# Performance work log

Hardware: AMD Instinct MI355X
Metric: run time of the kernel (lower is better)

## Reference

```python
import jax, jax.numpy as jnp
import numpy as np

D = H = W = 128
NUM_STEPS = 7  # MONAI DVF2DDF default


def _base_grid(dtype):
    zz, yy, xx = jnp.meshgrid(jnp.arange(D, dtype=dtype),
                              jnp.arange(H, dtype=dtype),
                              jnp.arange(W, dtype=dtype), indexing='ij')
    return jnp.stack([zz, yy, xx], 0)  # [3,D,H,W] voxel coords


def _warp(img, ddf, mode):
    # img: [1,C,D,H,W], ddf: [1,3,D,H,W] in voxel units.
    # Equivalent to grid_sample(align_corners=True, padding='border'):
    # border padding == clamp the voxel-space sample coordinate to [0, dim-1].
    dtype = ddf.dtype
    coords = _base_grid(dtype) + ddf[0]
    lims = jnp.array([D - 1, H - 1, W - 1], dtype=dtype).reshape(3, 1, 1, 1)
    coords = jnp.clip(coords, 0.0, lims)
    vol = img[0]  # [C,D,H,W]
    if mode == 'nearest':
        zi, yi, xi = jnp.round(coords).astype(jnp.int32)
        return vol[:, zi, yi, xi][None]
    z, y, x = coords
    z0 = jnp.floor(z); y0 = jnp.floor(y); x0 = jnp.floor(x)
    wz = z - z0; wy = y - y0; wx = x - x0
    z0i = z0.astype(jnp.int32); y0i = y0.astype(jnp.int32); x0i = x0.astype(jnp.int32)
    z1i = jnp.minimum(z0i + 1, D - 1)
    y1i = jnp.minimum(y0i + 1, H - 1)
    x1i = jnp.minimum(x0i + 1, W - 1)
    g = lambda a, b, c: vol[:, a, b, c]  # [C,D,H,W] gather
    out = (g(z0i, y0i, x0i) * (1 - wz) * (1 - wy) * (1 - wx)
         + g(z0i, y0i, x1i) * (1 - wz) * (1 - wy) * wx
         + g(z0i, y1i, x0i) * (1 - wz) * wy * (1 - wx)
         + g(z0i, y1i, x1i) * (1 - wz) * wy * wx
         + g(z1i, y0i, x0i) * wz * (1 - wy) * (1 - wx)
         + g(z1i, y0i, x1i) * wz * (1 - wy) * wx
         + g(z1i, y1i, x0i) * wz * wy * (1 - wx)
         + g(z1i, y1i, x1i) * wz * wy * wx)
    return out[None]


def _dvf2ddf(dvf):
    # scaling-and-squaring integration of a stationary velocity field
    ddf = dvf / (2.0 ** NUM_STEPS)
    for _ in range(NUM_STEPS):
        ddf = ddf + _warp(ddf, ddf, 'bilinear')
    return ddf


def setup_inputs() -> dict:
    key = jax.random.key(0)
    k1, k2, k3, k4 = jax.random.split(key, 4)
    dvf = jax.random.normal(k1, (1, 3, D, H, W), dtype=jnp.float32) * 0.5
    moving_image = jax.random.uniform(k2, (1, 1, D, H, W), dtype=jnp.float32)
    fixed_image = jax.random.uniform(k3, (1, 1, D, H, W), dtype=jnp.float32)
    moving_label = jax.random.randint(k4, (1, 1, D, H, W), 0, 4).astype(jnp.float32)
    return {'dvf': dvf, 'moving_image': moving_image,
            'fixed_image': fixed_image, 'moving_label': moving_label}


def reference(dvf, moving_image, fixed_image, moving_label):
    ddf = _dvf2ddf(dvf)
    pred_image = _warp(moving_image, ddf, 'bilinear')
    pred_label = _warp(moving_label, ddf, 'nearest')
    return (ddf, pred_image, pred_label, dvf)
```

## Files before the change

kernel.cpp:

```cpp
#include <hip/hip_runtime.h>

#define DD 128
constexpr int NV = DD * DD * DD;
constexpr float INV_SCALE = 1.0f / 128.0f;

__device__ __forceinline__ void unpack_zyx(int tid, int& z, int& y, int& x) {
    x = tid & (DD - 1);
    y = (tid >> 7) & (DD - 1);
    z = tid >> 14;
}

__device__ __forceinline__ float clampd(float v) {
    return fminf(fmaxf(v, 0.0f), (float)(DD - 1));
}

struct Corner {
    int i000, i001, i010, i011, i100, i101, i110, i111;
    float w000, w001, w010, w011, w100, w101, w110, w111;
};

__device__ __forceinline__ Corner make_corner(float cz, float cy, float cx) {
    Corner c;
    float z0f = floorf(cz), y0f = floorf(cy), x0f = floorf(cx);
    float wz = cz - z0f, wy = cy - y0f, wx = cx - x0f;
    int z0 = (int)z0f, y0 = (int)y0f, x0 = (int)x0f;
    int dx = (x0 < DD - 1) ? 1 : 0;
    int dy = (y0 < DD - 1) ? DD : 0;
    int dz = (z0 < DD - 1) ? DD * DD : 0;
    int i000 = (z0 << 14) + (y0 << 7) + x0;
    c.i000 = i000;           c.i001 = i000 + dx;
    c.i010 = i000 + dy;      c.i011 = i000 + dy + dx;
    c.i100 = i000 + dz;      c.i101 = i000 + dz + dx;
    c.i110 = i000 + dz + dy; c.i111 = i000 + dz + dy + dx;
    float omz = 1.0f - wz, omy = 1.0f - wy, omx = 1.0f - wx;
    c.w000 = omz * omy * omx; c.w001 = omz * omy * wx;
    c.w010 = omz * wy * omx;  c.w011 = omz * wy * wx;
    c.w100 = wz * omy * omx;  c.w101 = wz * omy * wx;
    c.w110 = wz * wy * omx;   c.w111 = wz * wy * wx;
    return c;
}


__global__ __launch_bounds__(256)
void init_step1_kernel(const float* __restrict__ dvf,
                       float4* __restrict__ dst,
                       float* __restrict__ dvf_out) {
    int tid = blockIdx.x * blockDim.x + threadIdx.x;
    int z, y, x;
    unpack_zyx(tid, z, y, x);

    float v0 = dvf[tid];
    float v1 = dvf[tid + NV];
    float v2 = dvf[tid + 2 * NV];

    dvf_out[tid]          = v0;
    dvf_out[tid + NV]     = v1;
    dvf_out[tid + 2 * NV] = v2;

    float d0 = v0 * INV_SCALE, d1 = v1 * INV_SCALE, d2 = v2 * INV_SCALE;

    float cz = clampd((float)z + d0);
    float cy = clampd((float)y + d1);
    float cx = clampd((float)x + d2);

    Corner c = make_corner(cz, cy, cx);
    const float* ch0 = dvf;
    const float* ch1 = dvf + NV;
    const float* ch2 = dvf + 2 * NV;

    float t0 = c.w000 * ch0[c.i000] + c.w001 * ch0[c.i001]
             + c.w010 * ch0[c.i010] + c.w011 * ch0[c.i011]
             + c.w100 * ch0[c.i100] + c.w101 * ch0[c.i101]
             + c.w110 * ch0[c.i110] + c.w111 * ch0[c.i111];
    float t1 = c.w000 * ch1[c.i000] + c.w001 * ch1[c.i001]
             + c.w010 * ch1[c.i010] + c.w011 * ch1[c.i011]
             + c.w100 * ch1[c.i100] + c.w101 * ch1[c.i101]
             + c.w110 * ch1[c.i110] + c.w111 * ch1[c.i111];
    float t2 = c.w000 * ch2[c.i000] + c.w001 * ch2[c.i001]
             + c.w010 * ch2[c.i010] + c.w011 * ch2[c.i011]
             + c.w100 * ch2[c.i100] + c.w101 * ch2[c.i101]
             + c.w110 * ch2[c.i110] + c.w111 * ch2[c.i111];

    dst[tid] = make_float4(t0 * INV_SCALE + d0,
                           t1 * INV_SCALE + d1,
                           t2 * INV_SCALE + d2, 0.0f);
}

template <bool PLANAR_OUT>
__global__ __launch_bounds__(256)
void step4_kernel(const float4* __restrict__ src,
                  float4* __restrict__ dst4,
                  float* __restrict__ dstp) {
    int tid = blockIdx.x * blockDim.x + threadIdx.x;
    int z, y, x;
    unpack_zyx(tid, z, y, x);

    float4 d = src[tid];

    float cz = clampd((float)z + d.x);
    float cy = clampd((float)y + d.y);
    float cx = clampd((float)x + d.z);

    Corner c = make_corner(cz, cy, cx);

    float4 v000 = src[c.i000], v001 = src[c.i001];
    float4 v010 = src[c.i010], v011 = src[c.i011];
    float4 v100 = src[c.i100], v101 = src[c.i101];
    float4 v110 = src[c.i110], v111 = src[c.i111];

    float r0 = c.w000 * v000.x + c.w001 * v001.x + c.w010 * v010.x + c.w011 * v011.x
             + c.w100 * v100.x + c.w101 * v101.x + c.w110 * v110.x + c.w111 * v111.x;
    float r1 = c.w000 * v000.y + c.w001 * v001.y + c.w010 * v010.y + c.w011 * v011.y
             + c.w100 * v100.y + c.w101 * v101.y + c.w110 * v110.y + c.w111 * v111.y;
    float r2 = c.w000 * v000.z + c.w001 * v001.z + c.w010 * v010.z + c.w011 * v011.z
             + c.w100 * v100.z + c.w101 * v101.z + c.w110 * v110.z + c.w111 * v111.z;

    r0 += d.x; r1 += d.y; r2 += d.z;

    if (PLANAR_OUT) {
        dstp[tid]          = r0;
        dstp[tid + NV]     = r1;
        dstp[tid + 2 * NV] = r2;
    } else {
        dst4[tid] = make_float4(r0, r1, r2, 0.0f);
    }
}

__global__ __launch_bounds__(256)
void final_kernel(const float* __restrict__ ddf,
                  const float* __restrict__ mimg,
                  const float* __restrict__ mlab,
                  float* __restrict__ pred_img,
                  float* __restrict__ pred_lab) {
    int tid = blockIdx.x * blockDim.x + threadIdx.x;
    int z, y, x;
    unpack_zyx(tid, z, y, x);

    float d0 = ddf[tid];
    float d1 = ddf[tid + NV];
    float d2 = ddf[tid + 2 * NV];

    float cz = clampd((float)z + d0);
    float cy = clampd((float)y + d1);
    float cx = clampd((float)x + d2);

    Corner c = make_corner(cz, cy, cx);

    float v = c.w000 * mimg[c.i000] + c.w001 * mimg[c.i001]
            + c.w010 * mimg[c.i010] + c.w011 * mimg[c.i011]
            + c.w100 * mimg[c.i100] + c.w101 * mimg[c.i101]
            + c.w110 * mimg[c.i110] + c.w111 * mimg[c.i111];
    pred_img[tid] = v;

    int zi = (int)rintf(cz);
    int yi = (int)rintf(cy);
    int xi = (int)rintf(cx);
    pred_lab[tid] = mlab[(zi << 14) + (yi << 7) + xi];
}


__device__ __forceinline__ void trilerp3(const float* __restrict__ src,
                                         float cz, float cy, float cx,
                                         float& r0, float& r1, float& r2) {
    Corner c = make_corner(cz, cy, cx);
    const float* p000 = src + 3 * c.i000;
    const float* p001 = src + 3 * c.i001;
    const float* p010 = src + 3 * c.i010;
    const float* p011 = src + 3 * c.i011;
    const float* p100 = src + 3 * c.i100;
    const float* p101 = src + 3 * c.i101;
    const float* p110 = src + 3 * c.i110;
    const float* p111 = src + 3 * c.i111;
    r0 = c.w000 * p000[0] + c.w001 * p001[0] + c.w010 * p010[0] + c.w011 * p011[0]
       + c.w100 * p100[0] + c.w101 * p101[0] + c.w110 * p110[0] + c.w111 * p111[0];
    r1 = c.w000 * p000[1] + c.w001 * p001[1] + c.w010 * p010[1] + c.w011 * p011[1]
       + c.w100 * p100[1] + c.w101 * p101[1] + c.w110 * p110[1] + c.w111 * p111[1];
    r2 = c.w000 * p000[2] + c.w001 * p001[2] + c.w010 * p010[2] + c.w011 * p011[2]
       + c.w100 * p100[2] + c.w101 * p101[2] + c.w110 * p110[2] + c.w111 * p111[2];
}

__global__ __launch_bounds__(256)
void init_kernel(const float* __restrict__ dvf, float* __restrict__ A) {
    int tid = blockIdx.x * blockDim.x + threadIdx.x;
    float d0 = dvf[tid] * INV_SCALE;
    float d1 = dvf[tid + NV] * INV_SCALE;
    float d2 = dvf[tid + 2 * NV] * INV_SCALE;
    float* p = A + 3 * tid;
    p[0] = d0; p[1] = d1; p[2] = d2;
}

template <bool PLANAR_OUT>
__global__ __launch_bounds__(256)
void step_kernel(const float* __restrict__ src, float* __restrict__ dst) {
    int tid = blockIdx.x * blockDim.x + threadIdx.x;
    int z, y, x;
    unpack_zyx(tid, z, y, x);
    const float* s = src + 3 * tid;
    float d0 = s[0], d1 = s[1], d2 = s[2];
    float cz = clampd((float)z + d0);
    float cy = clampd((float)y + d1);
    float cx = clampd((float)x + d2);
    float r0, r1, r2;
    trilerp3(src, cz, cy, cx, r0, r1, r2);
    r0 += d0; r1 += d1; r2 += d2;
    if (PLANAR_OUT) {
        dst[tid]          = r0;
        dst[tid + NV]     = r1;
        dst[tid + 2 * NV] = r2;
    } else {
        float* p = dst + 3 * tid;
        p[0] = r0; p[1] = r1; p[2] = r2;
    }
}

__global__ __launch_bounds__(256)
void final_kernel_fb(const float* __restrict__ ddf,
                     const float* __restrict__ mimg,
                     const float* __restrict__ mlab,
                     const float* __restrict__ dvf,
                     float* __restrict__ pred_img,
                     float* __restrict__ pred_lab,
                     float* __restrict__ dvf_out) {
    int tid = blockIdx.x * blockDim.x + threadIdx.x;
    int z, y, x;
    unpack_zyx(tid, z, y, x);
    float d0 = ddf[tid];
    float d1 = ddf[tid + NV];
    float d2 = ddf[tid + 2 * NV];
    float cz = clampd((float)z + d0);
    float cy = clampd((float)y + d1);
    float cx = clampd((float)x + d2);
    Corner c = make_corner(cz, cy, cx);
    float v = c.w000 * mimg[c.i000] + c.w001 * mimg[c.i001]
            + c.w010 * mimg[c.i010] + c.w011 * mimg[c.i011]
            + c.w100 * mimg[c.i100] + c.w101 * mimg[c.i101]
            + c.w110 * mimg[c.i110] + c.w111 * mimg[c.i111];
    pred_img[tid] = v;
    int zi = (int)rintf(cz);
    int yi = (int)rintf(cy);
    int xi = (int)rintf(cx);
    pred_lab[tid] = mlab[(zi << 14) + (yi << 7) + xi];
    dvf_out[tid]          = dvf[tid];
    dvf_out[tid + NV]     = dvf[tid + NV];
    dvf_out[tid + 2 * NV] = dvf[tid + 2 * NV];
}


extern "C" void kernel_launch(void* const* d_in, const int* in_sizes, int n_in,
                              void* d_out, int out_size, void* d_ws, size_t ws_size,
                              hipStream_t stream) {
    const float* dvf  = (const float*)d_in[0];
    const float* mimg = (const float*)d_in[1];
    const float* mlab = (const float*)d_in[3];

    float* out      = (float*)d_out;
    float* ddf_out  = out;
    float* pred_img = out + 3 * NV;
    float* pred_lab = out + 4 * NV;
    float* dvf_out  = out + 5 * NV;

    dim3 block(256);
    dim3 grid(NV / 256);

    size_t need = (size_t)2 * NV * sizeof(float4);
    if (d_ws != nullptr && ws_size >= need) {
        float4* A4 = (float4*)d_ws;
        float4* B4 = A4 + NV;
        init_step1_kernel<<<grid, block, 0, stream>>>(dvf, A4, dvf_out);
        step4_kernel<false><<<grid, block, 0, stream>>>(A4, B4, nullptr);
        step4_kernel<false><<<grid, block, 0, stream>>>(B4, A4, nullptr);
        step4_kernel<false><<<grid, block, 0, stream>>>(A4, B4, nullptr);
        step4_kernel<false><<<grid, block, 0, stream>>>(B4, A4, nullptr);
        step4_kernel<false><<<grid, block, 0, stream>>>(A4, B4, nullptr);
        step4_kernel<true ><<<grid, block, 0, stream>>>(B4, nullptr, ddf_out);
        final_kernel<<<grid, block, 0, stream>>>(ddf_out, mimg, mlab,
                                                 pred_img, pred_lab);
    } else {
        float* A = dvf_out;
        float* B = ddf_out;
        init_kernel<<<grid, block, 0, stream>>>(dvf, A);
        step_kernel<false><<<grid, block, 0, stream>>>(A, B);
        step_kernel<false><<<grid, block, 0, stream>>>(B, A);
        step_kernel<false><<<grid, block, 0, stream>>>(A, B);
        step_kernel<false><<<grid, block, 0, stream>>>(B, A);
        step_kernel<false><<<grid, block, 0, stream>>>(A, B);
        step_kernel<false><<<grid, block, 0, stream>>>(B, A);
        step_kernel<true ><<<grid, block, 0, stream>>>(A, B);
        final_kernel_fb<<<grid, block, 0, stream>>>(B, mimg, mlab, dvf,
                                                    pred_img, pred_lab, dvf_out);
    }
}
```

Before: 291.9 us.

## Stage displacement tiles with halo in shared memory for squaring steps

Replaces the per-voxel float4 gather step kernels with a tiled kernel. Each 16x8x8 block loads a halo-padded 22x14x14 region of the packed 3-channel field into LDS and does the trilinear gathers from there, falling back to global memory when a sample lands outside the halo. It also stops fusing the first step into init, so seven tiled steps now run, and it switches the workspace layout from float4 to packed float3. The aim is to cut scattered global and L2 gather traffic, at the cost of redundant halo loads, LDS bank conflicts from the stride-3 layout, and possible divergence on the fallback path.

```diff
diff --git a/kernel.cpp b/kernel.cpp
--- a/kernel.cpp
+++ b/kernel.cpp
@@ -14,24 +14,19 @@
     return fminf(fmaxf(v, 0.0f), (float)(DD - 1));
 }
 
-struct Corner {
-    int i000, i001, i010, i011, i100, i101, i110, i111;
+struct CornerW {
+    int x0, x1, y0, y1, z0, z1;
     float w000, w001, w010, w011, w100, w101, w110, w111;
 };
 
-__device__ __forceinline__ Corner make_corner(float cz, float cy, float cx) {
-    Corner c;
+__device__ __forceinline__ CornerW make_cornerw(float cz, float cy, float cx) {
+    CornerW c;
     float z0f = floorf(cz), y0f = floorf(cy), x0f = floorf(cx);
     float wz = cz - z0f, wy = cy - y0f, wx = cx - x0f;
-    int z0 = (int)z0f, y0 = (int)y0f, x0 = (int)x0f;
-    int dx = (x0 < DD - 1) ? 1 : 0;
-    int dy = (y0 < DD - 1) ? DD : 0;
-    int dz = (z0 < DD - 1) ? DD * DD : 0;
-    int i000 = (z0 << 14) + (y0 << 7) + x0;
-    c.i000 = i000;           c.i001 = i000 + dx;
-    c.i010 = i000 + dy;      c.i011 = i000 + dy + dx;
-    c.i100 = i000 + dz;      c.i101 = i000 + dz + dx;
-    c.i110 = i000 + dz + dy; c.i111 = i000 + dz + dy + dx;
+    c.z0 = (int)z0f; c.y0 = (int)y0f; c.x0 = (int)x0f;
+    c.z1 = min(c.z0 + 1, DD - 1);
+    c.y1 = min(c.y0 + 1, DD - 1);
+    c.x1 = min(c.x0 + 1, DD - 1);
     float omz = 1.0f - wz, omy = 1.0f - wy, omx = 1.0f - wx;
     c.w000 = omz * omy * omx; c.w001 = omz * omy * wx;
     c.w010 = omz * wy * omx;  c.w011 = omz * wy * wx;
@@ -42,87 +37,134 @@
 
 
 __global__ __launch_bounds__(256)
-void init_step1_kernel(const float* __restrict__ dvf,
-                       float4* __restrict__ dst,
+void init_fused_kernel(const float* __restrict__ dvf,
+                       float* __restrict__ A,
                        float* __restrict__ dvf_out) {
     int tid = blockIdx.x * blockDim.x + threadIdx.x;
-    int z, y, x;
-    unpack_zyx(tid, z, y, x);
-
     float v0 = dvf[tid];
     float v1 = dvf[tid + NV];
     float v2 = dvf[tid + 2 * NV];
-
     dvf_out[tid]          = v0;
     dvf_out[tid + NV]     = v1;
     dvf_out[tid + 2 * NV] = v2;
-
-    float d0 = v0 * INV_SCALE, d1 = v1 * INV_SCALE, d2 = v2 * INV_SCALE;
-
-    float cz = clampd((float)z + d0);
-    float cy = clampd((float)y + d1);
-    float cx = clampd((float)x + d2);
-
-    Corner c = make_corner(cz, cy, cx);
-    const float* ch0 = dvf;
-    const float* ch1 = dvf + NV;
-    const float* ch2 = dvf + 2 * NV;
-
-    float t0 = c.w000 * ch0[c.i000] + c.w001 * ch0[c.i001]
-             + c.w010 * ch0[c.i010] + c.w011 * ch0[c.i011]
-             + c.w100 * ch0[c.i100] + c.w101 * ch0[c.i101]
-             + c.w110 * ch0[c.i110] + c.w111 * ch0[c.i111];
-    float t1 = c.w000 * ch1[c.i000] + c.w001 * ch1[c.i001]
-             + c.w010 * ch1[c.i010] + c.w011 * ch1[c.i011]
-             + c.w100 * ch1[c.i100] + c.w101 * ch1[c.i101]
-             + c.w110 * ch1[c.i110] + c.w111 * ch1[c.i111];
-    float t2 = c.w000 * ch2[c.i000] + c.w001 * ch2[c.i001]
-             + c.w010 * ch2[c.i010] + c.w011 * ch2[c.i011]
-             + c.w100 * ch2[c.i100] + c.w101 * ch2[c.i101]
-             + c.w110 * ch2[c.i110] + c.w111 * ch2[c.i111];
-
-    dst[tid] = make_float4(t0 * INV_SCALE + d0,
-                           t1 * INV_SCALE + d1,
-                           t2 * INV_SCALE + d2, 0.0f);
-}
+    float* p = A + 3 * tid;
+    p[0] = v0 * INV_SCALE;
+    p[1] = v1 * INV_SCALE;
+    p[2] = v2 * INV_SCALE;
+}
+
+#define TX 16
+#define TY 8
+#define TZ 8
+#define HALO 3
+#define RX (TX + 6)
+#define RY (TY + 6)
+#define RZ (TZ + 6)
+constexpr int NCELLS = RX * RY * RZ;
 
 template <bool PLANAR_OUT>
 __global__ __launch_bounds__(256)
-void step4_kernel(const float4* __restrict__ src,
-                  float4* __restrict__ dst4,
-                  float* __restrict__ dstp) {
-    int tid = blockIdx.x * blockDim.x + threadIdx.x;
-    int z, y, x;
-    unpack_zyx(tid, z, y, x);
-
-    float4 d = src[tid];
-
-    float cz = clampd((float)z + d.x);
-    float cy = clampd((float)y + d.y);
-    float cx = clampd((float)x + d.z);
-
-    Corner c = make_corner(cz, cy, cx);
-
-    float4 v000 = src[c.i000], v001 = src[c.i001];
-    float4 v010 = src[c.i010], v011 = src[c.i011];
-    float4 v100 = src[c.i100], v101 = src[c.i101];
-    float4 v110 = src[c.i110], v111 = src[c.i111];
-
-    float r0 = c.w000 * v000.x + c.w001 * v001.x + c.w010 * v010.x + c.w011 * v011.x
-             + c.w100 * v100.x + c.w101 * v101.x + c.w110 * v110.x + c.w111 * v111.x;
-    float r1 = c.w000 * v000.y + c.w001 * v001.y + c.w010 * v010.y + c.w011 * v011.y
-             + c.w100 * v100.y + c.w101 * v101.y + c.w110 * v110.y + c.w111 * v111.y;
-    float r2 = c.w000 * v000.z + c.w001 * v001.z + c.w010 * v010.z + c.w011 * v011.z
-             + c.w100 * v100.z + c.w101 * v101.z + c.w110 * v110.z + c.w111 * v111.z;
-
-    r0 += d.x; r1 += d.y; r2 += d.z;
-
-    if (PLANAR_OUT) {
-        dstp[tid]          = r0;
-        dstp[tid + NV]     = r1;
-        dstp[tid + 2 * NV] = r2;
-    } else {
-        dst4[tid] = make_float4(r0, r1, r2, 0.0f);
+void tile_step_kernel(const float* __restrict__ src, float* __restrict__ dst) {
+    __shared__ float sf[NCELLS * 3];
+
+    int bid = blockIdx.x;
+    int bx = (bid & 7) * TX;
+    int by = ((bid >> 3) & 15) * TY;
+    int bz = (bid >> 7) * TZ;
+    int t = threadIdx.x;
+
+    for (int c = t; c < NCELLS; c += 256) {
+        int cx = c % RX;
+        int rem = c / RX;
+        int cy = rem % RY;
+        int cz = rem / RY;
+        int gx = min(max(bx - HALO + cx, 0), DD - 1);
+        int gy = min(max(by - HALO + cy, 0), DD - 1);
+        int gz = min(max(bz - HALO + cz, 0), DD - 1);
+        const float* p = src + 3 * ((gz << 14) + (gy << 7) + gx);
+        float a = p[0], b = p[1], d = p[2];
+        sf[3 * c]     = a;
+        sf[3 * c + 1] = b;
+        sf[3 * c + 2] = d;
+    }
+    __syncthreads();
+
+    #pragma unroll
+    for (int k = 0; k < 4; ++k) {
+        int v = t + k * 256;
+        int vx = v & (TX - 1);
+        int vy = (v >> 4) & (TY - 1);
+        int vz = v >> 7;
+        int x = bx + vx, y = by + vy, z = bz + vz;
+
+        int ocell = ((vz + HALO) * RY + (vy + HALO)) * RX + (vx + HALO);
+        float d0 = sf[3 * ocell];
+        float d1 = sf[3 * ocell + 1];
+        float d2 = sf[3 * ocell + 2];
+
+        float cz_ = clampd((float)z + d0);
+        float cy_ = clampd((float)y + d1);
+        float cx_ = clampd((float)x + d2);
+
+        CornerW c = make_cornerw(cz_, cy_, cx_);
+
+        int lx0 = c.x0 - bx + HALO, lx1 = c.x1 - bx + HALO;
+        int ly0 = c.y0 - by + HALO, ly1 = c.y1 - by + HALO;
+        int lz0 = c.z0 - bz + HALO, lz1 = c.z1 - bz + HALO;
+
+        float r0, r1, r2;
+        bool inl = (lx0 >= 0) & (lx1 <= RX - 1) &
+                   (ly0 >= 0) & (ly1 <= RY - 1) &
+                   (lz0 >= 0) & (lz1 <= RZ - 1);
+        if (inl) {
+            int r00 = (lz0 * RY + ly0) * RX;
+            int r01 = (lz0 * RY + ly1) * RX;
+            int r10 = (lz1 * RY + ly0) * RX;
+            int r11 = (lz1 * RY + ly1) * RX;
+            const float* p000 = sf + 3 * (r00 + lx0);
+            const float* p001 = sf + 3 * (r00 + lx1);
+            const float* p010 = sf + 3 * (r01 + lx0);
+            const float* p011 = sf + 3 * (r01 + lx1);
+            const float* p100 = sf + 3 * (r10 + lx0);
+            const float* p101 = sf + 3 * (r10 + lx1);
+            const float* p110 = sf + 3 * (r11 + lx0);
+            const float* p111 = sf + 3 * (r11 + lx1);
+            r0 = c.w000 * p000[0] + c.w001 * p001[0] + c.w010 * p010[0] + c.w011 * p011[0]
+               + c.w100 * p100[0] + c.w101 * p101[0] + c.w110 * p110[0] + c.w111 * p111[0];
+            r1 = c.w000 * p000[1] + c.w001 * p001[1] + c.w010 * p010[1] + c.w011 * p011[1]
+               + c.w100 * p100[1] + c.w101 * p101[1] + c.w110 * p110[1] + c.w111 * p111[1];
+            r2 = c.w000 * p000[2] + c.w001 * p001[2] + c.w010 * p010[2] + c.w011 * p011[2]
+               + c.w100 * p100[2] + c.w101 * p101[2] + c.w110 * p110[2] + c.w111 * p111[2];
+        } else {
+            int zs0 = c.z0 << 14, zs1 = c.z1 << 14;
+            int ys0 = c.y0 << 7,  ys1 = c.y1 << 7;
+            const float* p000 = src + 3 * (zs0 + ys0 + c.x0);
+            const float* p001 = src + 3 * (zs0 + ys0 + c.x1);
+            const float* p010 = src + 3 * (zs0 + ys1 + c.x0);
+            const float* p011 = src + 3 * (zs0 + ys1 + c.x1);
+            const float* p100 = src + 3 * (zs1 + ys0 + c.x0);
+            const float* p101 = src + 3 * (zs1 + ys0 + c.x1);
+            const float* p110 = src + 3 * (zs1 + ys1 + c.x0);
+            const float* p111 = src + 3 * (zs1 + ys1 + c.x1);
+            r0 = c.w000 * p000[0] + c.w001 * p001[0] + c.w010 * p010[0] + c.w011 * p011[0]
+               + c.w100 * p100[0] + c.w101 * p101[0] + c.w110 * p110[0] + c.w111 * p111[0];
+            r1 = c.w000 * p000[1] + c.w001 * p001[1] + c.w010 * p010[1] + c.w011 * p011[1]
+               + c.w100 * p100[1] + c.w101 * p101[1] + c.w110 * p110[1] + c.w111 * p111[1];
+            r2 = c.w000 * p000[2] + c.w001 * p001[2] + c.w010 * p010[2] + c.w011 * p011[2]
+               + c.w100 * p100[2] + c.w101 * p101[2] + c.w110 * p110[2] + c.w111 * p111[2];
+        }
+
+        r0 += d0; r1 += d1; r2 += d2;
+
+        int gid = (z << 14) + (y << 7) + x;
+        if (PLANAR_OUT) {
+            dst[gid]          = r0;
+            dst[gid + NV]     = r1;
+            dst[gid + 2 * NV] = r2;
+        } else {
+            float* p = dst + 3 * gid;
+            p[0] = r0; p[1] = r1; p[2] = r2;
+        }
     }
 }
 
@@ -144,12 +186,18 @@
     float cy = clampd((float)y + d1);
     float cx = clampd((float)x + d2);
 
-    Corner c = make_corner(cz, cy, cx);
-
-    float v = c.w000 * mimg[c.i000] + c.w001 * mimg[c.i001]
-            + c.w010 * mimg[c.i010] + c.w011 * mimg[c.i011]
-            + c.w100 * mimg[c.i100] + c.w101 * mimg[c.i101]
-            + c.w110 * mimg[c.i110] + c.w111 * mimg[c.i111];
+    CornerW c = make_cornerw(cz, cy, cx);
+    int zs0 = c.z0 << 14, zs1 = c.z1 << 14;
+    int ys0 = c.y0 << 7,  ys1 = c.y1 << 7;
+
+    float v = c.w000 * mimg[zs0 + ys0 + c.x0]
+            + c.w001 * mimg[zs0 + ys0 + c.x1]
+            + c.w010 * mimg[zs0 + ys1 + c.x0]
+            + c.w011 * mimg[zs0 + ys1 + c.x1]
+            + c.w100 * mimg[zs1 + ys0 + c.x0]
+            + c.w101 * mimg[zs1 + ys0 + c.x1]
+            + c.w110 * mimg[zs1 + ys1 + c.x0]
+            + c.w111 * mimg[zs1 + ys1 + c.x1];
     pred_img[tid] = v;
 
     int zi = (int)rintf(cz);
@@ -162,15 +210,17 @@
 __device__ __forceinline__ void trilerp3(const float* __restrict__ src,
                                          float cz, float cy, float cx,
                                          float& r0, float& r1, float& r2) {
-    Corner c = make_corner(cz, cy, cx);
-    const float* p000 = src + 3 * c.i000;
-    const float* p001 = src + 3 * c.i001;
-    const float* p010 = src + 3 * c.i010;
-    const float* p011 = src + 3 * c.i011;
-    const float* p100 = src + 3 * c.i100;
-    const float* p101 = src + 3 * c.i101;
-    const float* p110 = src + 3 * c.i110;
-    const float* p111 = src + 3 * c.i111;
+    CornerW c = make_cornerw(cz, cy, cx);
+    int zs0 = c.z0 << 14, zs1 = c.z1 << 14;
+    int ys0 = c.y0 << 7,  ys1 = c.y1 << 7;
+    const float* p000 = src + 3 * (zs0 + ys0 + c.x0);
+    const float* p001 = src + 3 * (zs0 + ys0 + c.x1);
+    const float* p010 = src + 3 * (zs0 + ys1 + c.x0);
+    const float* p011 = src + 3 * (zs0 + ys1 + c.x1);
+    const float* p100 = src + 3 * (zs1 + ys0 + c.x0);
+    const float* p101 = src + 3 * (zs1 + ys0 + c.x1);
+    const float* p110 = src + 3 * (zs1 + ys1 + c.x0);
+    const float* p111 = src + 3 * (zs1 + ys1 + c.x1);
     r0 = c.w000 * p000[0] + c.w001 * p001[0] + c.w010 * p010[0] + c.w011 * p011[0]
        + c.w100 * p100[0] + c.w101 * p101[0] + c.w110 * p110[0] + c.w111 * p111[0];
     r1 = c.w000 * p000[1] + c.w001 * p001[1] + c.w010 * p010[1] + c.w011 * p011[1]
@@ -230,11 +280,17 @@
     float cz = clampd((float)z + d0);
     float cy = clampd((float)y + d1);
     float cx = clampd((float)x + d2);
-    Corner c = make_corner(cz, cy, cx);
-    float v = c.w000 * mimg[c.i000] + c.w001 * mimg[c.i001]
-            + c.w010 * mimg[c.i010] + c.w011 * mimg[c.i011]
-            + c.w100 * mimg[c.i100] + c.w101 * mimg[c.i101]
-            + c.w110 * mimg[c.i110] + c.w111 * mimg[c.i111];
+    CornerW c = make_cornerw(cz, cy, cx);
+    int zs0 = c.z0 << 14, zs1 = c.z1 << 14;
+    int ys0 = c.y0 << 7,  ys1 = c.y1 << 7;
+    float v = c.w000 * mimg[zs0 + ys0 + c.x0]
+            + c.w001 * mimg[zs0 + ys0 + c.x1]
+            + c.w010 * mimg[zs0 + ys1 + c.x0]
+            + c.w011 * mimg[zs0 + ys1 + c.x1]
+            + c.w100 * mimg[zs1 + ys0 + c.x0]
+            + c.w101 * mimg[zs1 + ys0 + c.x1]
+            + c.w110 * mimg[zs1 + ys1 + c.x0]
+            + c.w111 * mimg[zs1 + ys1 + c.x1];
     pred_img[tid] = v;
     int zi = (int)rintf(cz);
     int yi = (int)rintf(cy);
@@ -261,18 +317,20 @@
 
     dim3 block(256);
     dim3 grid(NV / 256);
-
-    size_t need = (size_t)2 * NV * sizeof(float4);
+    dim3 tgrid(NV / 1024);
+
+    size_t need = (size_t)2 * NV * 3 * sizeof(float);
     if (d_ws != nullptr && ws_size >= need) {
-        float4* A4 = (float4*)d_ws;
-        float4* B4 = A4 + NV;
-        init_step1_kernel<<<grid, block, 0, stream>>>(dvf, A4, dvf_out);
-        step4_kernel<false><<<grid, block, 0, stream>>>(A4, B4, nullptr);
-        step4_kernel<false><<<grid, block, 0, stream>>>(B4, A4, nullptr);
-        step4_kernel<false><<<grid, block, 0, stream>>>(A4, B4, nullptr);
-        step4_kernel<false><<<grid, block, 0, stream>>>(B4, A4, nullptr);
-        step4_kernel<false><<<grid, block, 0, stream>>>(A4, B4, nullptr);
-        step4_kernel<true ><<<grid, block, 0, stream>>>(B4, nullptr, ddf_out);
+        float* A = (float*)d_ws;
+        float* B = A + (size_t)3 * NV;
+        init_fused_kernel<<<grid, block, 0, stream>>>(dvf, A, dvf_out);
+        tile_step_kernel<false><<<tgrid, block, 0, stream>>>(A, B);
+        tile_step_kernel<false><<<tgrid, block, 0, stream>>>(B, A);
+        tile_step_kernel<false><<<tgrid, block, 0, stream>>>(A, B);
+        tile_step_kernel<false><<<tgrid, block, 0, stream>>>(B, A);
+        tile_step_kernel<false><<<tgrid, block, 0, stream>>>(A, B);
+        tile_step_kernel<false><<<tgrid, block, 0, stream>>>(B, A);
+        tile_step_kernel<true ><<<tgrid, block, 0, stream>>>(A, ddf_out);
         final_kernel<<<grid, block, 0, stream>>>(ddf_out, mimg, mlab,
                                                  pred_img, pred_lab);
     } else {
```

Result: slower. 322.8 us (+10.6%).
